# Kernel optimization log

Hardware: AMD Instinct MI355X
Metric: run time of the kernel (lower is better)

## Reference

```python
import jax, jax.numpy as jnp
import numpy as np

D_MODEL = 300   # hardcoded d_model1 in Matposer.__init__
VOCAB = 32000
B, L = 512, 512
OUT = 4


def sinusoidal_pe(length, d):
    # Standard 'Attention is All You Need' positional encoding used by the repo's PositionalEncoding.
    pos = jnp.arange(length, dtype=jnp.float32)[:, None]
    div = jnp.exp(jnp.arange(0, d, 2, dtype=jnp.float32) * (-np.log(10000.0) / d))
    pe = jnp.zeros((length, d), dtype=jnp.float32)
    pe = pe.at[:, 0::2].set(jnp.sin(pos * div))
    pe = pe.at[:, 1::2].set(jnp.cos(pos * div))
    return pe


def setup_inputs() -> dict:
    key = jax.random.key(0)
    k1, k2, k3, k4, k5, k6 = jax.random.split(key, 6)
    return {
        "x1": jax.random.randint(k1, (B, L), 0, VOCAB, dtype=jnp.int32),
        "x2": jax.random.randint(k2, (B, L), 0, VOCAB, dtype=jnp.int32),
        "emb1": jax.random.normal(k3, (VOCAB, D_MODEL), dtype=jnp.float32) * 0.02,
        "emb2": jax.random.normal(k4, (VOCAB, D_MODEL), dtype=jnp.float32) * 0.02,
        "w1": jax.random.normal(k5, (D_MODEL, D_MODEL), dtype=jnp.float32) / np.sqrt(D_MODEL),
        "b1": jnp.zeros((D_MODEL,), dtype=jnp.float32),
        "w2": jax.random.normal(k6, (OUT, D_MODEL), dtype=jnp.float32) / np.sqrt(D_MODEL),
        "b2": jnp.zeros((OUT,), dtype=jnp.float32),
    }


def reference(x1, x2, emb1, emb2, w1, b1, w2, b2):
    scale = jnp.sqrt(jnp.float32(D_MODEL))   # Embeddings multiplies by sqrt(d_model)
    pe = sinusoidal_pe(x1.shape[1], D_MODEL)  # [L, D]
    # Embed + positional encoding (dropout=0 / eval mode). [B, L, D]
    e1 = emb1[x1] * scale + pe
    e2 = emb2[x2] * scale + pe
    # encoded_sents = e2.permute(0,2,1) @ e1 -> [B, D, D]
    fmap = jnp.einsum('bld,ble->bde', e2, e1)
    # torch Tensor.diagonal() defaults to dim1=0, dim2=1 -> shape [D, min(B, D)]
    diag = jnp.diagonal(fmap, axis1=0, axis2=1)  # [D, D] since B >= D
    # class_fc: Linear(300,300) -> ReLU -> Linear(300,output_size); torch Linear: x @ W.T + b
    h = jax.nn.relu(diag @ w1.T + b1)
    logits = h @ w2.T + b2
    # nn.Softmax() on a 2D input -> softmax over dim=1
    return jax.nn.softmax(logits, axis=-1)
```

## Files before the change

kernel.cpp:

```cpp
#include <hip/hip_runtime.h>
#include <math.h>

#define D_MODEL 300
#define LSEQ    512
#define NBATCH  300
#define SPLIT   8
#define LCH     (LSEQ / SPLIT)
#define NG      4
#define NR      75
#define KCH     (D_MODEL / 4)
#define JPB     2
#define SCALE   17.32050807568877f

__global__ void pe_kernel(float* __restrict__ pe) {
    int idx = blockIdx.x * blockDim.x + threadIdx.x;
    if (idx >= LSEQ * D_MODEL) return;
    int l = idx / D_MODEL;
    int e = idx - l * D_MODEL;
    int k = e >> 1;
    float dv = expf((float)(2 * k) * (-9.210340371976184f / 300.0f));
    float arg = (float)l * dv;
    pe[idx] = (e & 1) ? cosf(arg) : sinf(arg);
}

__global__ void diag_fused_kernel(const int* __restrict__ x1, const int* __restrict__ x2,
                                  const float* __restrict__ emb1, const float* __restrict__ emb2,
                                  const float* __restrict__ pe, float* __restrict__ Dm) {
    __shared__ int    x1ch[LCH];
    __shared__ float  sch[LCH];
    __shared__ float4 part[NG][NR];
    const int i   = blockIdx.x;
    const int sp  = blockIdx.y;
    const int tid = threadIdx.x;
    const int l0  = sp * LCH;

    if (tid < LCH) {
        const int l = l0 + tid;
        x1ch[tid] = x1[i * LSEQ + l];
        int idx2  = x2[i * LSEQ + l];
        sch[tid]  = emb2[idx2 * D_MODEL + i] * SCALE + pe[l * D_MODEL + i];
    }
    __syncthreads();

    const int g = tid / NR;
    const int r = tid - g * NR;

    if (tid < NG * NR) {
        float ax = 0.f, ay = 0.f, az = 0.f, aw = 0.f;
        #pragma unroll 4
        for (int l = g; l < LCH; l += NG) {
            const float4 ev = ((const float4*)(emb1 + (size_t)x1ch[l] * D_MODEL))[r];
            const float4 pv = ((const float4*)(pe   + (size_t)(l0 + l) * D_MODEL))[r];
            const float  s  = sch[l];
            ax = fmaf(s, fmaf(ev.x, SCALE, pv.x), ax);
            ay = fmaf(s, fmaf(ev.y, SCALE, pv.y), ay);
            az = fmaf(s, fmaf(ev.z, SCALE, pv.z), az);
            aw = fmaf(s, fmaf(ev.w, SCALE, pv.w), aw);
        }
        part[g][r] = make_float4(ax, ay, az, aw);
    }
    __syncthreads();

    if (g == 0 && tid < NR) {
        float4 p0 = part[0][r], p1 = part[1][r], p2 = part[2][r], p3 = part[3][r];
        float* dst = Dm + i * D_MODEL + 4 * r;
        atomicAdd(dst + 0, p0.x + p1.x + p2.x + p3.x);
        atomicAdd(dst + 1, p0.y + p1.y + p2.y + p3.y);
        atomicAdd(dst + 2, p0.z + p1.z + p2.z + p3.z);
        atomicAdd(dst + 3, p0.w + p1.w + p2.w + p3.w);
    }
}

__global__ void fc1_kernel(const float* __restrict__ w1, const float* __restrict__ Dm,
                           float* __restrict__ Hpre) {
    const int j0  = blockIdx.x * JPB;
    const int sp  = blockIdx.y;
    const int tid = threadIdx.x;
    const int k0  = sp * KCH;
    if (tid >= D_MODEL) return;
    const float* w1r0 = w1 + (j0 + 0) * D_MODEL + k0;
    const float* w1r1 = w1 + (j0 + 1) * D_MODEL + k0;
    float acc0 = 0.0f, acc1 = 0.0f;
    #pragma unroll 5
    for (int k = 0; k < KCH; ++k) {
        float d = Dm[(k0 + k) * D_MODEL + tid];
        acc0 = fmaf(w1r0[k], d, acc0);
        acc1 = fmaf(w1r1[k], d, acc1);
    }
    atomicAdd(&Hpre[(j0 + 0) * D_MODEL + tid], acc0);
    atomicAdd(&Hpre[(j0 + 1) * D_MODEL + tid], acc1);
}

__global__ void fc2_softmax_kernel(const float* __restrict__ Hpre, const float* __restrict__ b1,
                                   const float* __restrict__ w2, const float* __restrict__ b2,
                                   float* __restrict__ out) {
    __shared__ float sm[4][4][64];
    const int tid   = threadIdx.x;
    const int e_loc = tid & 63;
    const int jc    = tid >> 6;
    const int e     = blockIdx.x * 64 + e_loc;

    float a0 = 0.f, a1 = 0.f, a2 = 0.f, a3 = 0.f;
    if (e < D_MODEL) {
        const int j0 = jc * 75;
        #pragma unroll 5
        for (int j = j0; j < j0 + 75; ++j) {
            float h = fmaxf(Hpre[j * D_MODEL + e] + b1[j], 0.0f);
            a0 = fmaf(h, w2[0 * D_MODEL + j], a0);
            a1 = fmaf(h, w2[1 * D_MODEL + j], a1);
            a2 = fmaf(h, w2[2 * D_MODEL + j], a2);
            a3 = fmaf(h, w2[3 * D_MODEL + j], a3);
        }
    }
    sm[jc][0][e_loc] = a0; sm[jc][1][e_loc] = a1;
    sm[jc][2][e_loc] = a2; sm[jc][3][e_loc] = a3;
    __syncthreads();

    if (jc == 0 && e < D_MODEL) {
        float l0 = b2[0] + sm[0][0][e_loc] + sm[1][0][e_loc] + sm[2][0][e_loc] + sm[3][0][e_loc];
        float l1 = b2[1] + sm[0][1][e_loc] + sm[1][1][e_loc] + sm[2][1][e_loc] + sm[3][1][e_loc];
        float l2 = b2[2] + sm[0][2][e_loc] + sm[1][2][e_loc] + sm[2][2][e_loc] + sm[3][2][e_loc];
        float l3 = b2[3] + sm[0][3][e_loc] + sm[1][3][e_loc] + sm[2][3][e_loc] + sm[3][3][e_loc];
        float m  = fmaxf(fmaxf(l0, l1), fmaxf(l2, l3));
        float x0 = expf(l0 - m), x1 = expf(l1 - m), x2 = expf(l2 - m), x3 = expf(l3 - m);
        float inv = 1.0f / (x0 + x1 + x2 + x3);
        out[e * 4 + 0] = x0 * inv;
        out[e * 4 + 1] = x1 * inv;
        out[e * 4 + 2] = x2 * inv;
        out[e * 4 + 3] = x3 * inv;
    }
}

extern "C" void kernel_launch(void* const* d_in, const int* in_sizes, int n_in,
                              void* d_out, int out_size, void* d_ws, size_t ws_size,
                              hipStream_t stream) {
    const int*   x1   = (const int*)d_in[0];
    const int*   x2   = (const int*)d_in[1];
    const float* emb1 = (const float*)d_in[2];
    const float* emb2 = (const float*)d_in[3];
    const float* w1   = (const float*)d_in[4];
    const float* b1   = (const float*)d_in[5];
    const float* w2   = (const float*)d_in[6];
    const float* b2   = (const float*)d_in[7];
    float* out = (float*)d_out;

    char* ws = (char*)d_ws;
    float* pe   = (float*)ws;
    float* Dm   = (float*)(ws + 614400);
    float* Hpre = (float*)(ws + 974400);

    (void)hipMemsetAsync(Dm, 0, 2 * 360000, stream);

    pe_kernel<<<(LSEQ * D_MODEL + 255) / 256, 256, 0, stream>>>(pe);
    diag_fused_kernel<<<dim3(NBATCH, SPLIT), 320, 0, stream>>>(x1, x2, emb1, emb2, pe, Dm);
    fc1_kernel<<<dim3(D_MODEL / JPB, 4), 320, 0, stream>>>(w1, Dm, Hpre);
    fc2_softmax_kernel<<<(D_MODEL + 63) / 64, 256, 0, stream>>>(Hpre, b1, w2, b2, out);
}
```

Measured before the change: 157.6 us.

## Split diagonal contraction into embedding term and shared positional-encoding term

The diagonal computation is split algebraically: Dm[i] = sum_l s_l*(scale*emb1 + pe) becomes a scaled-embedding gather term plus a separate s^T·pe matrix product that reuses pe across six batches per block from shared memory. A new pass precomputes S (the emb2 diagonal element plus pe) once, and the gather kernel now only reads emb1 rows, with a fully unrolled 8-row load per group and a doubled L split. This removes the per-row pe reads from the gather loop, at the cost of two extra launches, an extra buffer and more atomics.

```diff
diff --git a/kernel.cpp b/kernel.cpp
--- a/kernel.cpp
+++ b/kernel.cpp
@@ -4,12 +4,14 @@
 #define D_MODEL 300
 #define LSEQ    512
 #define NBATCH  300
-#define SPLIT   8
+#define SPLIT   16
 #define LCH     (LSEQ / SPLIT)
 #define NG      4
+#define LPG     (LCH / NG)
 #define NR      75
 #define KCH     (D_MODEL / 4)
 #define JPB     2
+#define TI      6
 #define SCALE   17.32050807568877f
 
 __global__ void pe_kernel(float* __restrict__ pe) {
@@ -23,9 +25,18 @@
     pe[idx] = (e & 1) ? cosf(arg) : sinf(arg);
 }
 
-__global__ void diag_fused_kernel(const int* __restrict__ x1, const int* __restrict__ x2,
-                                  const float* __restrict__ emb1, const float* __restrict__ emb2,
-                                  const float* __restrict__ pe, float* __restrict__ Dm) {
+__global__ void s_kernel(const int* __restrict__ x2, const float* __restrict__ emb2,
+                         const float* __restrict__ pe, float* __restrict__ S) {
+    int idx = blockIdx.x * blockDim.x + threadIdx.x;
+    if (idx >= NBATCH * LSEQ) return;
+    int i = idx >> 9;
+    int l = idx & (LSEQ - 1);
+    int v = x2[idx];
+    S[idx] = emb2[(size_t)v * D_MODEL + i] * SCALE + pe[l * D_MODEL + i];
+}
+
+__global__ void diagA_kernel(const int* __restrict__ x1, const float* __restrict__ S,
+                             const float* __restrict__ emb1, float* __restrict__ Dm) {
     __shared__ int    x1ch[LCH];
     __shared__ float  sch[LCH];
     __shared__ float4 part[NG][NR];
@@ -35,10 +46,8 @@
     const int l0  = sp * LCH;
 
     if (tid < LCH) {
-        const int l = l0 + tid;
-        x1ch[tid] = x1[i * LSEQ + l];
-        int idx2  = x2[i * LSEQ + l];
-        sch[tid]  = emb2[idx2 * D_MODEL + i] * SCALE + pe[l * D_MODEL + i];
+        x1ch[tid] = x1[i * LSEQ + l0 + tid];
+        sch[tid]  = S[i * LSEQ + l0 + tid] * SCALE;
     }
     __syncthreads();
 
@@ -46,17 +55,26 @@
     const int r = tid - g * NR;
 
     if (tid < NG * NR) {
-        float ax = 0.f, ay = 0.f, az = 0.f, aw = 0.f;
-        #pragma unroll 4
-        for (int l = g; l < LCH; l += NG) {
-            const float4 ev = ((const float4*)(emb1 + (size_t)x1ch[l] * D_MODEL))[r];
-            const float4 pv = ((const float4*)(pe   + (size_t)(l0 + l) * D_MODEL))[r];
-            const float  s  = sch[l];
-            ax = fmaf(s, fmaf(ev.x, SCALE, pv.x), ax);
-            ay = fmaf(s, fmaf(ev.y, SCALE, pv.y), ay);
-            az = fmaf(s, fmaf(ev.z, SCALE, pv.z), az);
-            aw = fmaf(s, fmaf(ev.w, SCALE, pv.w), aw);
-        }
+        const int lb = g * LPG;
+        const float4 v0 = ((const float4*)(emb1 + (size_t)x1ch[lb + 0] * D_MODEL))[r];
+        const float4 v1 = ((const float4*)(emb1 + (size_t)x1ch[lb + 1] * D_MODEL))[r];
+        const float4 v2 = ((const float4*)(emb1 + (size_t)x1ch[lb + 2] * D_MODEL))[r];
+        const float4 v3 = ((const float4*)(emb1 + (size_t)x1ch[lb + 3] * D_MODEL))[r];
+        const float4 v4 = ((const float4*)(emb1 + (size_t)x1ch[lb + 4] * D_MODEL))[r];
+        const float4 v5 = ((const float4*)(emb1 + (size_t)x1ch[lb + 5] * D_MODEL))[r];
+        const float4 v6 = ((const float4*)(emb1 + (size_t)x1ch[lb + 6] * D_MODEL))[r];
+        const float4 v7 = ((const float4*)(emb1 + (size_t)x1ch[lb + 7] * D_MODEL))[r];
+        const float s0 = sch[lb + 0], s1 = sch[lb + 1], s2 = sch[lb + 2], s3 = sch[lb + 3];
+        const float s4 = sch[lb + 4], s5 = sch[lb + 5], s6 = sch[lb + 6], s7 = sch[lb + 7];
+        float ax, ay, az, aw;
+        ax = s0 * v0.x;            ay = s0 * v0.y;            az = s0 * v0.z;            aw = s0 * v0.w;
+        ax = fmaf(s1, v1.x, ax);   ay = fmaf(s1, v1.y, ay);   az = fmaf(s1, v1.z, az);   aw = fmaf(s1, v1.w, aw);
+        ax = fmaf(s2, v2.x, ax);   ay = fmaf(s2, v2.y, ay);   az = fmaf(s2, v2.z, az);   aw = fmaf(s2, v2.w, aw);
+        ax = fmaf(s3, v3.x, ax);   ay = fmaf(s3, v3.y, ay);   az = fmaf(s3, v3.z, az);   aw = fmaf(s3, v3.w, aw);
+        ax = fmaf(s4, v4.x, ax);   ay = fmaf(s4, v4.y, ay);   az = fmaf(s4, v4.z, az);   aw = fmaf(s4, v4.w, aw);
+        ax = fmaf(s5, v5.x, ax);   ay = fmaf(s5, v5.y, ay);   az = fmaf(s5, v5.z, az);   aw = fmaf(s5, v5.w, aw);
+        ax = fmaf(s6, v6.x, ax);   ay = fmaf(s6, v6.y, ay);   az = fmaf(s6, v6.z, az);   aw = fmaf(s6, v6.w, aw);
+        ax = fmaf(s7, v7.x, ax);   ay = fmaf(s7, v7.y, ay);   az = fmaf(s7, v7.z, az);   aw = fmaf(s7, v7.w, aw);
         part[g][r] = make_float4(ax, ay, az, aw);
     }
     __syncthreads();
@@ -68,6 +86,48 @@
         atomicAdd(dst + 1, p0.y + p1.y + p2.y + p3.y);
         atomicAdd(dst + 2, p0.z + p1.z + p2.z + p3.z);
         atomicAdd(dst + 3, p0.w + p1.w + p2.w + p3.w);
+    }
+}
+
+__global__ void termB_kernel(const float* __restrict__ S, const float* __restrict__ pe,
+                             float* __restrict__ Dm) {
+    __shared__ float sS[TI][LSEQ];
+    const int i0  = blockIdx.x * TI;
+    const int tid = threadIdx.x;
+
+    for (int t = tid; t < TI * LSEQ; t += 320) {
+        int ti = t >> 9;
+        int l  = t & (LSEQ - 1);
+        sS[ti][l] = S[(i0 + ti) * LSEQ + l];
+    }
+    __syncthreads();
+
+    if (tid < D_MODEL) {
+        float acc0 = 0.f, acc1 = 0.f, acc2 = 0.f, acc3 = 0.f, acc4 = 0.f, acc5 = 0.f;
+        for (int l = 0; l < LSEQ; l += 4) {
+            float p0 = pe[(l + 0) * D_MODEL + tid];
+            float p1 = pe[(l + 1) * D_MODEL + tid];
+            float p2 = pe[(l + 2) * D_MODEL + tid];
+            float p3 = pe[(l + 3) * D_MODEL + tid];
+            acc0 = fmaf(sS[0][l + 0], p0, acc0); acc0 = fmaf(sS[0][l + 1], p1, acc0);
+            acc0 = fmaf(sS[0][l + 2], p2, acc0); acc0 = fmaf(sS[0][l + 3], p3, acc0);
+            acc1 = fmaf(sS[1][l + 0], p0, acc1); acc1 = fmaf(sS[1][l + 1], p1, acc1);
+            acc1 = fmaf(sS[1][l + 2], p2, acc1); acc1 = fmaf(sS[1][l + 3], p3, acc1);
+            acc2 = fmaf(sS[2][l + 0], p0, acc2); acc2 = fmaf(sS[2][l + 1], p1, acc2);
+            acc2 = fmaf(sS[2][l + 2], p2, acc2); acc2 = fmaf(sS[2][l + 3], p3, acc2);
+            acc3 = fmaf(sS[3][l + 0], p0, acc3); acc3 = fmaf(sS[3][l + 1], p1, acc3);
+            acc3 = fmaf(sS[3][l + 2], p2, acc3); acc3 = fmaf(sS[3][l + 3], p3, acc3);
+            acc4 = fmaf(sS[4][l + 0], p0, acc4); acc4 = fmaf(sS[4][l + 1], p1, acc4);
+            acc4 = fmaf(sS[4][l + 2], p2, acc4); acc4 = fmaf(sS[4][l + 3], p3, acc4);
+            acc5 = fmaf(sS[5][l + 0], p0, acc5); acc5 = fmaf(sS[5][l + 1], p1, acc5);
+            acc5 = fmaf(sS[5][l + 2], p2, acc5); acc5 = fmaf(sS[5][l + 3], p3, acc5);
+        }
+        atomicAdd(&Dm[(i0 + 0) * D_MODEL + tid], acc0);
+        atomicAdd(&Dm[(i0 + 1) * D_MODEL + tid], acc1);
+        atomicAdd(&Dm[(i0 + 2) * D_MODEL + tid], acc2);
+        atomicAdd(&Dm[(i0 + 3) * D_MODEL + tid], acc3);
+        atomicAdd(&Dm[(i0 + 4) * D_MODEL + tid], acc4);
+        atomicAdd(&Dm[(i0 + 5) * D_MODEL + tid], acc5);
     }
 }
 
@@ -148,11 +208,14 @@
     float* pe   = (float*)ws;
     float* Dm   = (float*)(ws + 614400);
     float* Hpre = (float*)(ws + 974400);
+    float* S    = (float*)(ws + 1334400);
 
     (void)hipMemsetAsync(Dm, 0, 2 * 360000, stream);
 
     pe_kernel<<<(LSEQ * D_MODEL + 255) / 256, 256, 0, stream>>>(pe);
-    diag_fused_kernel<<<dim3(NBATCH, SPLIT), 320, 0, stream>>>(x1, x2, emb1, emb2, pe, Dm);
+    s_kernel<<<(NBATCH * LSEQ + 255) / 256, 256, 0, stream>>>(x2, emb2, pe, S);
+    diagA_kernel<<<dim3(NBATCH, SPLIT), 320, 0, stream>>>(x1, S, emb1, Dm);
+    termB_kernel<<<NBATCH / TI, 320, 0, stream>>>(S, pe, Dm);
     fc1_kernel<<<dim3(D_MODEL / JPB, 4), 320, 0, stream>>>(w1, Dm, Hpre);
     fc2_softmax_kernel<<<(D_MODEL + 63) / 64, 256, 0, stream>>>(Hpre, b1, w2, b2, out);
 }
```

After: 205.5 us. +30.4%, slower.

## Compute positional encoding inline and drop separate PE kernel and buffer

Applied to the files above, without the earlier changes.

Removes the PE precompute kernel and its global buffer. The sinusoidal terms are now computed on the fly with fast __sinf/__cosf/__expf intrinsics inside the diagonal kernel. The split across L is doubled, and each thread issues 8 independent embedding gathers up front to expose more memory-level parallelism. The cost is extra transcendental ALU work per element and reduced accuracy from the fast intrinsics at large arguments, plus twice as many atomic adds.

```diff
diff --git a/kernel.cpp b/kernel.cpp
--- a/kernel.cpp
+++ b/kernel.cpp
@@ -4,28 +4,20 @@
 #define D_MODEL 300
 #define LSEQ    512
 #define NBATCH  300
-#define SPLIT   8
+#define SPLIT   16
 #define LCH     (LSEQ / SPLIT)
 #define NG      4
+#define LPG     (LCH / NG)
 #define NR      75
 #define KCH     (D_MODEL / 4)
 #define JPB     2
 #define SCALE   17.32050807568877f
+#define C2      0.030701134573253947f
+#define PIH     1.5707963267948966f
 
-__global__ void pe_kernel(float* __restrict__ pe) {
-    int idx = blockIdx.x * blockDim.x + threadIdx.x;
-    if (idx >= LSEQ * D_MODEL) return;
-    int l = idx / D_MODEL;
-    int e = idx - l * D_MODEL;
-    int k = e >> 1;
-    float dv = expf((float)(2 * k) * (-9.210340371976184f / 300.0f));
-    float arg = (float)l * dv;
-    pe[idx] = (e & 1) ? cosf(arg) : sinf(arg);
-}
-
-__global__ void diag_fused_kernel(const int* __restrict__ x1, const int* __restrict__ x2,
-                                  const float* __restrict__ emb1, const float* __restrict__ emb2,
-                                  const float* __restrict__ pe, float* __restrict__ Dm) {
+__global__ void diagAB_kernel(const int* __restrict__ x1, const int* __restrict__ x2,
+                              const float* __restrict__ emb1, const float* __restrict__ emb2,
+                              float* __restrict__ Dm) {
     __shared__ int    x1ch[LCH];
     __shared__ float  sch[LCH];
     __shared__ float4 part[NG][NR];
@@ -37,8 +29,10 @@
     if (tid < LCH) {
         const int l = l0 + tid;
         x1ch[tid] = x1[i * LSEQ + l];
-        int idx2  = x2[i * LSEQ + l];
-        sch[tid]  = emb2[idx2 * D_MODEL + i] * SCALE + pe[l * D_MODEL + i];
+        const int v2 = x2[i * LSEQ + l];
+        const float dvi = __expf(-C2 * (float)(i & ~1));
+        const float arg = (float)l * dvi + ((i & 1) ? PIH : 0.0f);
+        sch[tid] = fmaf(emb2[(size_t)v2 * D_MODEL + i], SCALE, __sinf(arg));
     }
     __syncthreads();
 
@@ -46,16 +40,41 @@
     const int r = tid - g * NR;
 
     if (tid < NG * NR) {
-        float ax = 0.f, ay = 0.f, az = 0.f, aw = 0.f;
-        #pragma unroll 4
-        for (int l = g; l < LCH; l += NG) {
-            const float4 ev = ((const float4*)(emb1 + (size_t)x1ch[l] * D_MODEL))[r];
-            const float4 pv = ((const float4*)(pe   + (size_t)(l0 + l) * D_MODEL))[r];
-            const float  s  = sch[l];
-            ax = fmaf(s, fmaf(ev.x, SCALE, pv.x), ax);
-            ay = fmaf(s, fmaf(ev.y, SCALE, pv.y), ay);
-            az = fmaf(s, fmaf(ev.z, SCALE, pv.z), az);
-            aw = fmaf(s, fmaf(ev.w, SCALE, pv.w), aw);
+        const int lb = g * LPG;
+        const float4 v0 = ((const float4*)(emb1 + (size_t)x1ch[lb + 0] * D_MODEL))[r];
+        const float4 v1 = ((const float4*)(emb1 + (size_t)x1ch[lb + 1] * D_MODEL))[r];
+        const float4 v2 = ((const float4*)(emb1 + (size_t)x1ch[lb + 2] * D_MODEL))[r];
+        const float4 v3 = ((const float4*)(emb1 + (size_t)x1ch[lb + 3] * D_MODEL))[r];
+        const float4 v4 = ((const float4*)(emb1 + (size_t)x1ch[lb + 4] * D_MODEL))[r];
+        const float4 v5 = ((const float4*)(emb1 + (size_t)x1ch[lb + 5] * D_MODEL))[r];
+        const float4 v6 = ((const float4*)(emb1 + (size_t)x1ch[lb + 6] * D_MODEL))[r];
+        const float4 v7 = ((const float4*)(emb1 + (size_t)x1ch[lb + 7] * D_MODEL))[r];
+        const float s0 = sch[lb + 0], s1 = sch[lb + 1], s2 = sch[lb + 2], s3 = sch[lb + 3];
+        const float s4 = sch[lb + 4], s5 = sch[lb + 5], s6 = sch[lb + 6], s7 = sch[lb + 7];
+        const float t0 = s0 * SCALE, t1 = s1 * SCALE, t2 = s2 * SCALE, t3 = s3 * SCALE;
+        const float t4 = s4 * SCALE, t5 = s5 * SCALE, t6 = s6 * SCALE, t7 = s7 * SCALE;
+        float ax, ay, az, aw;
+        ax = t0 * v0.x;            ay = t0 * v0.y;            az = t0 * v0.z;            aw = t0 * v0.w;
+        ax = fmaf(t1, v1.x, ax);   ay = fmaf(t1, v1.y, ay);   az = fmaf(t1, v1.z, az);   aw = fmaf(t1, v1.w, aw);
+        ax = fmaf(t2, v2.x, ax);   ay = fmaf(t2, v2.y, ay);   az = fmaf(t2, v2.z, az);   aw = fmaf(t2, v2.w, aw);
+        ax = fmaf(t3, v3.x, ax);   ay = fmaf(t3, v3.y, ay);   az = fmaf(t3, v3.z, az);   aw = fmaf(t3, v3.w, aw);
+        ax = fmaf(t4, v4.x, ax);   ay = fmaf(t4, v4.y, ay);   az = fmaf(t4, v4.z, az);   aw = fmaf(t4, v4.w, aw);
+        ax = fmaf(t5, v5.x, ax);   ay = fmaf(t5, v5.y, ay);   az = fmaf(t5, v5.z, az);   aw = fmaf(t5, v5.w, aw);
+        ax = fmaf(t6, v6.x, ax);   ay = fmaf(t6, v6.y, ay);   az = fmaf(t6, v6.z, az);   aw = fmaf(t6, v6.w, aw);
+        ax = fmaf(t7, v7.x, ax);   ay = fmaf(t7, v7.y, ay);   az = fmaf(t7, v7.z, az);   aw = fmaf(t7, v7.w, aw);
+
+        const float dvA = __expf(-C2 * (float)(4 * r));
+        const float dvB = __expf(-C2 * (float)(4 * r + 2));
+        const float s8[LPG] = {s0, s1, s2, s3, s4, s5, s6, s7};
+        #pragma unroll
+        for (int q = 0; q < LPG; ++q) {
+            const float fl = (float)(l0 + lb + q);
+            const float aA = fl * dvA;
+            const float aB = fl * dvB;
+            ax = fmaf(s8[q], __sinf(aA), ax);
+            ay = fmaf(s8[q], __cosf(aA), ay);
+            az = fmaf(s8[q], __sinf(aB), az);
+            aw = fmaf(s8[q], __cosf(aB), aw);
         }
         part[g][r] = make_float4(ax, ay, az, aw);
     }
@@ -145,14 +164,12 @@
     float* out = (float*)d_out;
 
     char* ws = (char*)d_ws;
-    float* pe   = (float*)ws;
-    float* Dm   = (float*)(ws + 614400);
-    float* Hpre = (float*)(ws + 974400);
+    float* Dm   = (float*)ws;
+    float* Hpre = (float*)(ws + 360000);
 
     (void)hipMemsetAsync(Dm, 0, 2 * 360000, stream);
 
-    pe_kernel<<<(LSEQ * D_MODEL + 255) / 256, 256, 0, stream>>>(pe);
-    diag_fused_kernel<<<dim3(NBATCH, SPLIT), 320, 0, stream>>>(x1, x2, emb1, emb2, pe, Dm);
+    diagAB_kernel<<<dim3(NBATCH, SPLIT), 320, 0, stream>>>(x1, x2, emb1, emb2, Dm);
     fc1_kernel<<<dim3(D_MODEL / JPB, 4), 320, 0, stream>>>(w1, Dm, Hpre);
     fc2_softmax_kernel<<<(D_MODEL + 63) / 64, 256, 0, stream>>>(Hpre, b1, w2, b2, out);
 }
```

Result: no change. 154.9 us (median of 2 runs) (-1.7%).

## Sort gather entries by vocab row and scatter into shared-memory partials

Applied to the files above, without the earlier changes.

Replaces the per-batch gather of emb1 rows with a counting sort of (token, batch, scale) entries by vocabulary id, so each emb1 row is read in sorted order and its contributions are scattered via LDS atomics into per-block partial Dm tiles that a separate kernel reduces. The positional-encoding contribution is split into its own kernel computed analytically with sin, and the precomputed pe buffer is removed. This trades the random emb1 row gathers for extra passes (count, scan, fill with global atomics, partial write/reduce of about 23 MB) and shared-memory atomic contention. It also uses __sinf/__expf approximations, which may lose accuracy.

```diff
diff --git a/kernel.cpp b/kernel.cpp
--- a/kernel.cpp
+++ b/kernel.cpp
@@ -4,70 +4,154 @@
 #define D_MODEL 300
 #define LSEQ    512
 #define NBATCH  300
-#define SPLIT   8
-#define LCH     (LSEQ / SPLIT)
-#define NG      4
-#define NR      75
-#define KCH     (D_MODEL / 4)
+#define VOCAB   32000
+#define NENT    (NBATCH * LSEQ)
+#define KCH     75
+#define ECH     4
+#define NBLK    64
+#define EPB     (NENT / NBLK)
+#define TI      6
 #define JPB     2
 #define SCALE   17.32050807568877f
-
-__global__ void pe_kernel(float* __restrict__ pe) {
-    int idx = blockIdx.x * blockDim.x + threadIdx.x;
-    if (idx >= LSEQ * D_MODEL) return;
-    int l = idx / D_MODEL;
-    int e = idx - l * D_MODEL;
-    int k = e >> 1;
-    float dv = expf((float)(2 * k) * (-9.210340371976184f / 300.0f));
-    float arg = (float)l * dv;
-    pe[idx] = (e & 1) ? cosf(arg) : sinf(arg);
-}
-
-__global__ void diag_fused_kernel(const int* __restrict__ x1, const int* __restrict__ x2,
-                                  const float* __restrict__ emb1, const float* __restrict__ emb2,
-                                  const float* __restrict__ pe, float* __restrict__ Dm) {
-    __shared__ int    x1ch[LCH];
-    __shared__ float  sch[LCH];
-    __shared__ float4 part[NG][NR];
-    const int i   = blockIdx.x;
-    const int sp  = blockIdx.y;
+#define C2      0.030701134573253947f
+#define PIH     1.5707963267948966f
+
+__global__ void count_kernel(const int* __restrict__ x1, int* __restrict__ cnt) {
+    int idx = blockIdx.x * 256 + threadIdx.x;
+    if (idx < NENT) atomicAdd(&cnt[x1[idx]], 1);
+}
+
+__global__ __launch_bounds__(1024) void scan_kernel(const int* __restrict__ cnt,
+                                                    int* __restrict__ cur) {
+    __shared__ int lds[1024];
+    const int t = threadIdx.x;
+    const int v0 = t * 32;
+    int local[32];
+    int tot = 0;
+    #pragma unroll
+    for (int k = 0; k < 32; ++k) {
+        int v = v0 + k;
+        int c = (v < VOCAB) ? cnt[v] : 0;
+        local[k] = tot;
+        tot += c;
+    }
+    lds[t] = tot;
+    __syncthreads();
+    int mysum = tot;
+    for (int d = 1; d < 1024; d <<= 1) {
+        int add = (t >= d) ? lds[t - d] : 0;
+        __syncthreads();
+        lds[t] += add;
+        __syncthreads();
+    }
+    int base = lds[t] - mysum;
+    #pragma unroll
+    for (int k = 0; k < 32; ++k) {
+        int v = v0 + k;
+        if (v < VOCAB) cur[v] = base + local[k];
+    }
+}
+
+__global__ void fill_kernel(const int* __restrict__ x1, const int* __restrict__ x2,
+                            const float* __restrict__ emb2, int* __restrict__ cur,
+                            int2* __restrict__ entries) {
+    int idx = blockIdx.x * 256 + threadIdx.x;
+    if (idx >= NENT) return;
+    int i = idx >> 9, l = idx & (LSEQ - 1);
+    int v = x1[idx];
+    float dvi = __expf(-C2 * (float)(i & ~1));
+    float arg = (float)l * dvi + ((i & 1) ? PIH : 0.0f);
+    float S = fmaf(emb2[(size_t)x2[idx] * D_MODEL + i], SCALE, __sinf(arg));
+    int pos = atomicAdd(&cur[v], 1);
+    entries[pos] = make_int2((v << 9) | i, __float_as_int(SCALE * S));
+}
+
+__global__ __launch_bounds__(512) void scatter_kernel(const float* __restrict__ emb1,
+                                                      const int2* __restrict__ entries,
+                                                      float* __restrict__ P) {
+    __shared__ float acc[NBATCH * KCH];
     const int tid = threadIdx.x;
-    const int l0  = sp * LCH;
-
-    if (tid < LCH) {
-        const int l = l0 + tid;
-        x1ch[tid] = x1[i * LSEQ + l];
-        int idx2  = x2[i * LSEQ + l];
-        sch[tid]  = emb2[idx2 * D_MODEL + i] * SCALE + pe[l * D_MODEL + i];
-    }
-    __syncthreads();
-
-    const int g = tid / NR;
-    const int r = tid - g * NR;
-
-    if (tid < NG * NR) {
-        float ax = 0.f, ay = 0.f, az = 0.f, aw = 0.f;
-        #pragma unroll 4
-        for (int l = g; l < LCH; l += NG) {
-            const float4 ev = ((const float4*)(emb1 + (size_t)x1ch[l] * D_MODEL))[r];
-            const float4 pv = ((const float4*)(pe   + (size_t)(l0 + l) * D_MODEL))[r];
-            const float  s  = sch[l];
-            ax = fmaf(s, fmaf(ev.x, SCALE, pv.x), ax);
-            ay = fmaf(s, fmaf(ev.y, SCALE, pv.y), ay);
-            az = fmaf(s, fmaf(ev.z, SCALE, pv.z), az);
-            aw = fmaf(s, fmaf(ev.w, SCALE, pv.w), aw);
+    const int bx  = blockIdx.x;
+    const int ec  = blockIdx.y;
+    const int e0  = ec * KCH;
+
+    for (int p = tid; p < NBATCH * KCH; p += 512) acc[p] = 0.0f;
+    __syncthreads();
+
+    if (tid < 450) {
+        const int g    = tid / 75;
+        const int lane = tid - g * 75;
+        const float* e1l = emb1 + e0 + lane;
+        const int base = bx * EPB + g;
+        for (int m = 0; m < EPB / 6; m += 4) {
+            const int2 q0 = entries[base + 6 * (m + 0)];
+            const int2 q1 = entries[base + 6 * (m + 1)];
+            const int2 q2 = entries[base + 6 * (m + 2)];
+            const int2 q3 = entries[base + 6 * (m + 3)];
+            const float r0 = e1l[(size_t)(q0.x >> 9) * D_MODEL];
+            const float r1 = e1l[(size_t)(q1.x >> 9) * D_MODEL];
+            const float r2 = e1l[(size_t)(q2.x >> 9) * D_MODEL];
+            const float r3 = e1l[(size_t)(q3.x >> 9) * D_MODEL];
+            atomicAdd(&acc[(q0.x & 511) * KCH + lane], __int_as_float(q0.y) * r0);
+            atomicAdd(&acc[(q1.x & 511) * KCH + lane], __int_as_float(q1.y) * r1);
+            atomicAdd(&acc[(q2.x & 511) * KCH + lane], __int_as_float(q2.y) * r2);
+            atomicAdd(&acc[(q3.x & 511) * KCH + lane], __int_as_float(q3.y) * r3);
         }
-        part[g][r] = make_float4(ax, ay, az, aw);
-    }
-    __syncthreads();
-
-    if (g == 0 && tid < NR) {
-        float4 p0 = part[0][r], p1 = part[1][r], p2 = part[2][r], p3 = part[3][r];
-        float* dst = Dm + i * D_MODEL + 4 * r;
-        atomicAdd(dst + 0, p0.x + p1.x + p2.x + p3.x);
-        atomicAdd(dst + 1, p0.y + p1.y + p2.y + p3.y);
-        atomicAdd(dst + 2, p0.z + p1.z + p2.z + p3.z);
-        atomicAdd(dst + 3, p0.w + p1.w + p2.w + p3.w);
+    }
+    __syncthreads();
+
+    float* myP = P + (size_t)(ec * NBLK + bx) * (NBATCH * KCH);
+    for (int p = tid; p < NBATCH * KCH; p += 512) myP[p] = acc[p];
+}
+
+__global__ void reduce_kernel(const float* __restrict__ P, float* __restrict__ Dm) {
+    const int p  = blockIdx.x * 256 + threadIdx.x;
+    const int ec = blockIdx.y;
+    if (p >= NBATCH * KCH) return;
+    float s = 0.0f;
+    #pragma unroll 8
+    for (int b = 0; b < NBLK; ++b)
+        s += P[(size_t)(ec * NBLK + b) * (NBATCH * KCH) + p];
+    const int i = p / KCH, c = p - i * KCH;
+    Dm[i * D_MODEL + ec * KCH + c] = s;
+}
+
+__global__ void termB_kernel(const int* __restrict__ x2, const float* __restrict__ emb2,
+                             float* __restrict__ Dm) {
+    __shared__ float sS[TI][64];
+    const int i0  = blockIdx.x * TI;
+    const int l0  = blockIdx.y * 64;
+    const int tid = threadIdx.x;
+
+    for (int t = tid; t < TI * 64; t += 320) {
+        const int ti = t >> 6, lr = t & 63;
+        const int gi = i0 + ti, gl = l0 + lr;
+        const float dvi = __expf(-C2 * (float)(gi & ~1));
+        const float arg = (float)gl * dvi + ((gi & 1) ? PIH : 0.0f);
+        sS[ti][lr] = fmaf(emb2[(size_t)x2[gi * LSEQ + gl] * D_MODEL + gi], SCALE, __sinf(arg));
+    }
+    __syncthreads();
+
+    if (tid < D_MODEL) {
+        const float dv = __expf(-C2 * (float)(tid & ~1));
+        const float ph = (tid & 1) ? PIH : 0.0f;
+        float a0 = 0.f, a1 = 0.f, a2 = 0.f, a3 = 0.f, a4 = 0.f, a5 = 0.f;
+        #pragma unroll 8
+        for (int l = 0; l < 64; ++l) {
+            const float pv = __sinf((float)(l0 + l) * dv + ph);
+            a0 = fmaf(sS[0][l], pv, a0);
+            a1 = fmaf(sS[1][l], pv, a1);
+            a2 = fmaf(sS[2][l], pv, a2);
+            a3 = fmaf(sS[3][l], pv, a3);
+            a4 = fmaf(sS[4][l], pv, a4);
+            a5 = fmaf(sS[5][l], pv, a5);
+        }
+        atomicAdd(&Dm[(i0 + 0) * D_MODEL + tid], a0);
+        atomicAdd(&Dm[(i0 + 1) * D_MODEL + tid], a1);
+        atomicAdd(&Dm[(i0 + 2) * D_MODEL + tid], a2);
+        atomicAdd(&Dm[(i0 + 3) * D_MODEL + tid], a3);
+        atomicAdd(&Dm[(i0 + 4) * D_MODEL + tid], a4);
+        atomicAdd(&Dm[(i0 + 5) * D_MODEL + tid], a5);
     }
 }
 
@@ -145,14 +229,21 @@
     float* out = (float*)d_out;
 
     char* ws = (char*)d_ws;
-    float* pe   = (float*)ws;
-    float* Dm   = (float*)(ws + 614400);
-    float* Hpre = (float*)(ws + 974400);
-
-    (void)hipMemsetAsync(Dm, 0, 2 * 360000, stream);
-
-    pe_kernel<<<(LSEQ * D_MODEL + 255) / 256, 256, 0, stream>>>(pe);
-    diag_fused_kernel<<<dim3(NBATCH, SPLIT), 320, 0, stream>>>(x1, x2, emb1, emb2, pe, Dm);
-    fc1_kernel<<<dim3(D_MODEL / JPB, 4), 320, 0, stream>>>(w1, Dm, Hpre);
+    int*   cnt     = (int*)ws;
+    float* Hpre    = (float*)(ws + 128000);
+    int*   cur     = (int*)(ws + 488000);
+    int2*  entries = (int2*)(ws + 616000);
+    float* P       = (float*)(ws + 1844800);
+    float* Dm      = (float*)(ws + 24884800);
+
+    (void)hipMemsetAsync(ws, 0, 488000, stream);
+
+    count_kernel<<<(NENT + 255) / 256, 256, 0, stream>>>(x1, cnt);
+    scan_kernel<<<1, 1024, 0, stream>>>(cnt, cur);
+    fill_kernel<<<(NENT + 255) / 256, 256, 0, stream>>>(x1, x2, emb2, cur, entries);
+    scatter_kernel<<<dim3(NBLK, ECH), 512, 0, stream>>>(emb1, entries, P);
+    reduce_kernel<<<dim3((NBATCH * KCH + 255) / 256, ECH), 256, 0, stream>>>(P, Dm);
+    termB_kernel<<<dim3(NBATCH / TI, LSEQ / 64), 320, 0, stream>>>(x2, emb2, Dm);
+    fc1_kernel<<<dim3(D_MODEL / JPB, ECH), 320, 0, stream>>>(w1, Dm, Hpre);
     fc2_softmax_kernel<<<(D_MODEL + 63) / 64, 256, 0, stream>>>(Hpre, b1, w2, b2, out);
 }
```

New measurement: 418.9 us. +165.8%, slower.
